# Performance work log

Measured on AMD Instinct MI355X. Metric: run time of the kernel, lower is better.

## Reference

```python
import jax, jax.numpy as jnp
import numpy as np

B, M, L, IN_C, MID_C, OUT_C = 1, 128, 256, 256, 32, 128


def setup_inputs() -> dict:
    key = jax.random.key(0)
    k_x, k_proj, k_final = jax.random.split(key, 3)
    return {
        "x1d": jax.random.normal(k_x, (B, M, L, IN_C), dtype=jnp.float32),
        "norm_w": jnp.ones((IN_C,), dtype=jnp.float32),
        "norm_b": jnp.zeros((IN_C,), dtype=jnp.float32),
        "proj_w": jax.random.normal(k_proj, (2 * MID_C, IN_C), dtype=jnp.float32) * 0.02,
        "proj_b": jnp.zeros((2 * MID_C,), dtype=jnp.float32),
        "final_w": jax.random.normal(k_final, (OUT_C, MID_C * MID_C), dtype=jnp.float32) * 0.02,
        "final_b": jnp.zeros((OUT_C,), dtype=jnp.float32),
    }


def reference(x1d, norm_w, norm_b, proj_w, proj_b, final_w, final_b):
    # LayerNorm over channel dim
    mu = jnp.mean(x1d, axis=-1, keepdims=True)
    var = jnp.mean(jnp.square(x1d - mu), axis=-1, keepdims=True)
    x = (x1d - mu) * jax.lax.rsqrt(var + 1e-5) * norm_w + norm_b

    mid_c = proj_w.shape[0] // 2
    # Linear -> (b, m, L, 2*mid_c); view (..., mid_c, 2); chunk & squeeze:
    # i = interleaved even channels, j = interleaved odd channels
    p = jnp.einsum('bmlc,dc->bmld', x, proj_w) + proj_b
    p = p.reshape(*p.shape[:-1], mid_c, 2)
    i, j = p[..., 0], p[..., 1]          # each (b, m, L, mid_c)

    m = x1d.shape[1]
    # Outer product mean over the MSA (m) dimension -> (b, L, L, mid_c, mid_c)
    x2d = jnp.einsum('bmix,bmjy->bijxy', i, j) / m

    b, li, lj = x2d.shape[0], x2d.shape[1], x2d.shape[2]
    flat = x2d.reshape(b, li, lj, mid_c * mid_c)
    out = jnp.einsum('bijf,of->bijo', flat, final_w) + final_b
    return out
```

## Files before the change

### kernel.cpp

```cpp
#include <hip/hip_runtime.h>
#include <hip/hip_bf16.h>

#define DEVINL __device__ __forceinline__

typedef float  f32x4_t  __attribute__((ext_vector_type(4)));
typedef float  f32x16_t __attribute__((ext_vector_type(16)));
typedef short  bf16x8_t __attribute__((ext_vector_type(8)));

#define MFMA16(a,b,c) __builtin_amdgcn_mfma_f32_16x16x32_bf16((a),(b),(c),0,0,0)
#define MFMA32(a,b,c) __builtin_amdgcn_mfma_f32_32x32x16_bf16((a),(b),(c),0,0,0)

DEVINL unsigned short f2bf(float f) {
  union { float f; unsigned u; } v; v.f = f;
  unsigned r = v.u + 0x7fffu + ((v.u >> 16) & 1u);
  return (unsigned short)(r >> 16);
}

DEVINL unsigned pk2bf(float lo, float hi) {
  union { __hip_bfloat162 h2; unsigned u; } v;
  v.h2 = __float22bfloat162_rn(make_float2(lo, hi));
  return v.u;
}


__global__ __launch_bounds__(256) void kA(const float* __restrict__ x,
                                          const float* __restrict__ nw,
                                          const float* __restrict__ nb,
                                          const float* __restrict__ pw,
                                          const float* __restrict__ pb,
                                          const float* __restrict__ fw,
                                          unsigned short* __restrict__ Wb,
                                          unsigned short* __restrict__ Ig,
                                          unsigned short* __restrict__ Jg) {
  if (blockIdx.x >= 1024) {
    int T = (blockIdx.x - 1024) * 256 + threadIdx.x;
    int o     = T >> 8;
    int kpos0 = (T & 255) * 4;
    int y  = kpos0 >> 5;
    int x0 = kpos0 & 31;
    const float* fo = fw + o * 1024 + y;
    ushort4 u;
    u.x = f2bf(fo[(x0 + 0) * 32]);
    u.y = f2bf(fo[(x0 + 1) * 32]);
    u.z = f2bf(fo[(x0 + 2) * 32]);
    u.w = f2bf(fo[(x0 + 3) * 32]);
    size_t off = (size_t)((o >> 5) * 64 + (kpos0 >> 4)) * 512 + (o & 31) * 16
               + ((kpos0 >> 3) & 1) * 8 + (kpos0 & 7);
    *(ushort4*)&Wb[off] = u;
    return;
  }
  __shared__ unsigned short xnl[32 * 264];
  __shared__ unsigned short pwl[64 * 264];
  __shared__ unsigned short ep[64 * 36];
  const int tid  = threadIdx.x;
  const int wv   = tid >> 6;
  const int lane = tid & 63;
  const int q    = lane >> 4;
  const int ln16 = lane & 15;
  const int l    = blockIdx.x & 255;
  const int m0   = (blockIdx.x >> 8) * 32;

  const float4* xs = (const float4*)x;
  float4 v[8];
#pragma unroll
  for (int i = 0; i < 8; i++) {
    int row = m0 + i * 4 + wv;
    v[i] = xs[row * 16384 + l * 64 + lane];
  }
  float4 nw4 = ((const float4*)nw)[lane];
  float4 nb4 = ((const float4*)nb)[lane];

#pragma unroll
  for (int i = 0; i < 8; i++) {
    float s  = v[i].x + v[i].y + v[i].z + v[i].w;
    float ss = v[i].x * v[i].x + v[i].y * v[i].y + v[i].z * v[i].z + v[i].w * v[i].w;
#pragma unroll
    for (int off = 32; off > 0; off >>= 1) {
      s  += __shfl_xor(s, off);
      ss += __shfl_xor(ss, off);
    }
    float mu  = s * (1.0f / 256.0f);
    float var = ss * (1.0f / 256.0f) - mu * mu;
    float rs  = rsqrtf(var + 1e-5f);
    ushort4 u;
    u.x = f2bf((v[i].x - mu) * rs * nw4.x + nb4.x);
    u.y = f2bf((v[i].y - mu) * rs * nw4.y + nb4.y);
    u.z = f2bf((v[i].z - mu) * rs * nw4.z + nb4.z);
    u.w = f2bf((v[i].w - mu) * rs * nw4.w + nb4.w);
    *(ushort4*)&xnl[(i * 4 + wv) * 264 + lane * 4] = u;
  }

  const float4* ps = (const float4*)pw;
#pragma unroll
  for (int i = 0; i < 16; i++) {
    float4 w4 = ps[i * 256 + tid];
    ushort4 u;
    u.x = f2bf(w4.x); u.y = f2bf(w4.y); u.z = f2bf(w4.z); u.w = f2bf(w4.w);
    *(ushort4*)&pwl[(i * 4 + wv) * 264 + lane * 4] = u;
  }
  __syncthreads();

  const int rt = wv & 1;
  const int db = (wv >> 1) * 32;
  f32x4_t acc[2] = {{0.f, 0.f, 0.f, 0.f}, {0.f, 0.f, 0.f, 0.f}};
#pragma unroll
  for (int kc = 0; kc < 8; kc++) {
    bf16x8_t a  = *(const bf16x8_t*)&xnl[(rt * 16 + ln16) * 264 + kc * 32 + q * 8];
    bf16x8_t b0 = *(const bf16x8_t*)&pwl[(db + ln16) * 264 + kc * 32 + q * 8];
    bf16x8_t b1 = *(const bf16x8_t*)&pwl[(db + 16 + ln16) * 264 + kc * 32 + q * 8];
    acc[0] = MFMA16(a, b0, acc[0]);
    acc[1] = MFMA16(a, b1, acc[1]);
  }

#pragma unroll
  for (int t2 = 0; t2 < 2; t2++) {
    int d = db + t2 * 16 + ln16;
    float bias  = pb[d];
    float scale = (d & 1) ? 1.0f : (1.0f / 128.0f);
#pragma unroll
    for (int r = 0; r < 4; r++) {
      int mloc = rt * 16 + q * 4 + r;
      ep[d * 36 + mloc] = f2bf((acc[t2][r] + bias) * scale);
    }
  }
  __syncthreads();

  const int h  = tid >> 3;
  const int m4 = tid & 7;
  const size_t off = (size_t)(l * 8 + (m0 >> 4) + (m4 >> 2)) * 512 + h * 16 + ((m4 >> 1) & 1) * 8 + (m4 & 1) * 4;
  ushort4 vi = *(const ushort4*)&ep[(2 * h) * 36 + m4 * 4];
  *(ushort4*)&Ig[off] = vi;
  ushort4 vj = *(const ushort4*)&ep[(2 * h + 1) * 36 + m4 * 4];
  *(ushort4*)&Jg[off] = vj;
}

__global__ __launch_bounds__(512, 2) void kB(const unsigned short* __restrict__ Ig,
                                             const unsigned short* __restrict__ Jg,
                                             const unsigned short* __restrict__ Wb,
                                             const float* __restrict__ fb,
                                             float* __restrict__ out) {
  extern __shared__ unsigned short fl[];
  constexpr int P = 1048;
  const int tid  = threadIdx.x;
  const int w    = tid >> 6;
  const int lane = tid & 63;
  const int ln32 = lane & 31;
  const int h    = lane >> 5;
  const int p    = blockIdx.x >> 4;
  const int t    = blockIdx.x & 15;

  bf16x8_t jb[2][8];
  const size_t jbase = (size_t)(t * 16 + 2 * w) * 4096 + ln32 * 16 + h * 8;
#pragma unroll
  for (int mc = 0; mc < 8; mc++) jb[0][mc] = *(const bf16x8_t*)&Jg[jbase + mc * 512];
#pragma unroll
  for (int mc = 0; mc < 8; mc++) jb[1][mc] = *(const bf16x8_t*)&Jg[jbase + 4096 + mc * 512];

#pragma unroll
  for (int s = 0; s < 2; s++) {
    const int jl = 2 * w + s;
#pragma unroll
    for (int ilp = 0; ilp < 2; ilp++) {
      bf16x8_t af[2][8];
#pragma unroll
      for (int u = 0; u < 2; u++)
#pragma unroll
        for (int mc = 0; mc < 8; mc++)
          af[u][mc] = *(const bf16x8_t*)&Ig[(size_t)((p * 4 + ilp * 2 + u) * 8 + mc) * 512 + ln32 * 16 + h * 8];
      f32x16_t c[2];
#pragma unroll
      for (int i = 0; i < 16; i++) { c[0][i] = 0.f; c[1][i] = 0.f; }
#pragma unroll
      for (int mc = 0; mc < 8; mc++) {
        c[0] = MFMA32(af[0][mc], jb[s][mc], c[0]);
        c[1] = MFMA32(af[1][mc], jb[s][mc], c[1]);
      }
#pragma unroll
      for (int u = 0; u < 2; u++) {
        unsigned short* fr = &fl[((ilp * 2 + u) * 16 + jl) * P];
#pragma unroll
        for (int g = 0; g < 4; g++) {
          int cp = (4 * ln32 + g) ^ (ln32 & 7);
          uint2 pv;
          pv.x = pk2bf(c[u][4 * g + 0], c[u][4 * g + 1]);
          pv.y = pk2bf(c[u][4 * g + 2], c[u][4 * g + 3]);
          *(uint2*)&fr[cp * 8 + h * 4] = pv;
        }
      }
    }
  }

  const int ot = w & 3;
  const int kh = w >> 2;
  const unsigned short* Wp = Wb + (size_t)(ot * 64 + kh * 32) * 512 + ln32 * 16 + h * 8;
  bf16x8_t bq[4];
  bq[0] = *(const bf16x8_t*)&Wp[0];
  bq[1] = *(const bf16x8_t*)&Wp[512];

  __syncthreads();

  bq[2] = *(const bf16x8_t*)&Wp[2 * 512];
  bq[3] = *(const bf16x8_t*)&Wp[3 * 512];

#define LDA(rt, kc) (*(const bf16x8_t*)&fl[((rt) * 32 + ln32) * P + \
    ((((kh * 32 + (kc)) * 2 + h) ^ (((kh * 32 + (kc)) >> 1) & 7)) * 8)])

  f32x16_t o2[2];
#pragma unroll
  for (int i = 0; i < 16; i++) { o2[0][i] = 0.f; o2[1][i] = 0.f; }

  bf16x8_t a0 = LDA(0, 0), a1 = LDA(1, 0);
#pragma unroll
  for (int kc = 0; kc < 32; kc++) {
    bf16x8_t ac0 = a0, ac1 = a1, bc = bq[kc & 3];
    if (kc < 31) { a0 = LDA(0, kc + 1); a1 = LDA(1, kc + 1); }
    if (kc < 28) bq[kc & 3] = *(const bf16x8_t*)&Wp[(kc + 4) * 512];
    o2[0] = MFMA32(ac0, bc, o2[0]);
    o2[1] = MFMA32(ac1, bc, o2[1]);
  }
#undef LDA

  __syncthreads();
  float* red = (float*)fl;
  if (kh == 1) {
#pragma unroll
    for (int rt = 0; rt < 2; rt++) {
      float* bb = red + (ot * 2 + rt) * 1024 + lane * 2;
#pragma unroll
      for (int k = 0; k < 8; k++)
        *(float2*)&bb[k * 128] = make_float2(o2[rt][2 * k], o2[rt][2 * k + 1]);
    }
  }
  __syncthreads();
  if (kh == 0) {
    const float bias = fb[ot * 32 + ln32];
    float* ob = out + ((size_t)(p * 4) * 256 + t * 16) * 128 + ot * 32 + ln32;
#pragma unroll
    for (int rt = 0; rt < 2; rt++) {
      const float* bb = red + (ot * 2 + rt) * 1024 + lane * 2;
#pragma unroll
      for (int k = 0; k < 8; k++) {
        float2 rv = *(const float2*)&bb[k * 128];
        int r0 = 2 * k, r1 = 2 * k + 1;
        int br0 = rt * 32 + (r0 & 3) + 8 * (r0 >> 2) + 4 * h;
        int br1 = rt * 32 + (r1 & 3) + 8 * (r1 >> 2) + 4 * h;
        ob[(br0 >> 4) * 32768 + (br0 & 15) * 128] = o2[rt][r0] + rv.x + bias;
        ob[(br1 >> 4) * 32768 + (br1 & 15) * 128] = o2[rt][r1] + rv.y + bias;
      }
    }
  }
}

extern "C" void kernel_launch(void* const* d_in, const int* in_sizes, int n_in,
                              void* d_out, int out_size, void* d_ws, size_t ws_size,
                              hipStream_t stream) {
  const float* x1d     = (const float*)d_in[0];
  const float* norm_w  = (const float*)d_in[1];
  const float* norm_b  = (const float*)d_in[2];
  const float* proj_w  = (const float*)d_in[3];
  const float* proj_b  = (const float*)d_in[4];
  const float* final_w = (const float*)d_in[5];
  const float* final_b = (const float*)d_in[6];
  float* outp          = (float*)d_out;

  unsigned short* Wb  = (unsigned short*)d_ws;
  unsigned short* Igp = Wb + 131072;
  unsigned short* Jgp = Igp + 1048576;

  const int kb_lds = 64 * 1048 * 2;
  hipFuncSetAttribute((const void*)kB, hipFuncAttributeMaxDynamicSharedMemorySize, kb_lds);

  kA<<<1152, 256, 0, stream>>>(x1d, norm_w, norm_b, proj_w, proj_b, final_w, Wb, Igp, Jgp);
  kB<<<1024, 512, kb_lds, stream>>>(Igp, Jgp, Wb, final_b, outp);
}
```

Before: 136.8 us.

## Split outer-product stage by j parity to overlap with final projection GEMM

The first GEMM (outer product into shared memory) is split into even and odd j halves, with a barrier between them. The final-projection GEMM on the even half can then start while other warps finish the odd half, instead of waiting behind a single barrier. The second GEMM's warp split moves from 4 output tiles × 2 K halves to 2 output pairs × 4 K quarters. Each A fragment read from LDS now feeds two MFMAs, which cuts LDS traffic per MFMA. In exchange there are more barriers, a 4-way cross-warp reduction through shared memory, and more live accumulator registers.

Measured after the change: 156.4 us. 1.14x slower.

```diff
diff --git a/kernel.cpp b/kernel.cpp
--- a/kernel.cpp
+++ b/kernel.cpp
@@ -149,16 +149,10 @@
   const int p    = blockIdx.x >> 4;
   const int t    = blockIdx.x & 15;
 
-  bf16x8_t jb[2][8];
-  const size_t jbase = (size_t)(t * 16 + 2 * w) * 4096 + ln32 * 16 + h * 8;
-#pragma unroll
-  for (int mc = 0; mc < 8; mc++) jb[0][mc] = *(const bf16x8_t*)&Jg[jbase + mc * 512];
-#pragma unroll
-  for (int mc = 0; mc < 8; mc++) jb[1][mc] = *(const bf16x8_t*)&Jg[jbase + 4096 + mc * 512];
-
-#pragma unroll
-  for (int s = 0; s < 2; s++) {
-    const int jl = 2 * w + s;
+  const unsigned short* Ibase = Ig + (size_t)(p * 32) * 512 + ln32 * 16 + h * 8;
+  const unsigned short* Jb    = Jg + (size_t)(t * 16) * 4096 + ln32 * 16 + h * 8;
+
+  auto gemm1 = [&](int jl, const bf16x8_t* jb) {
 #pragma unroll
     for (int ilp = 0; ilp < 2; ilp++) {
       bf16x8_t af[2][8];
@@ -166,14 +160,14 @@
       for (int u = 0; u < 2; u++)
 #pragma unroll
         for (int mc = 0; mc < 8; mc++)
-          af[u][mc] = *(const bf16x8_t*)&Ig[(size_t)((p * 4 + ilp * 2 + u) * 8 + mc) * 512 + ln32 * 16 + h * 8];
+          af[u][mc] = *(const bf16x8_t*)&Ibase[(size_t)((ilp * 2 + u) * 8 + mc) * 512];
       f32x16_t c[2];
 #pragma unroll
       for (int i = 0; i < 16; i++) { c[0][i] = 0.f; c[1][i] = 0.f; }
 #pragma unroll
       for (int mc = 0; mc < 8; mc++) {
-        c[0] = MFMA32(af[0][mc], jb[s][mc], c[0]);
-        c[1] = MFMA32(af[1][mc], jb[s][mc], c[1]);
+        c[0] = MFMA32(af[0][mc], jb[mc], c[0]);
+        c[1] = MFMA32(af[1][mc], jb[mc], c[1]);
       }
 #pragma unroll
       for (int u = 0; u < 2; u++) {
@@ -188,66 +182,104 @@
         }
       }
     }
-  }
-
-  const int ot = w & 3;
-  const int kh = w >> 2;
-  const unsigned short* Wp = Wb + (size_t)(ot * 64 + kh * 32) * 512 + ln32 * 16 + h * 8;
-  bf16x8_t bq[4];
-  bq[0] = *(const bf16x8_t*)&Wp[0];
-  bq[1] = *(const bf16x8_t*)&Wp[512];
-
-  __syncthreads();
-
-  bq[2] = *(const bf16x8_t*)&Wp[2 * 512];
-  bq[3] = *(const bf16x8_t*)&Wp[3 * 512];
-
-#define LDA(rt, kc) (*(const bf16x8_t*)&fl[((rt) * 32 + ln32) * P + \
-    ((((kh * 32 + (kc)) * 2 + h) ^ (((kh * 32 + (kc)) >> 1) & 7)) * 8)])
-
-  f32x16_t o2[2];
-#pragma unroll
-  for (int i = 0; i < 16; i++) { o2[0][i] = 0.f; o2[1][i] = 0.f; }
-
-  bf16x8_t a0 = LDA(0, 0), a1 = LDA(1, 0);
-#pragma unroll
-  for (int kc = 0; kc < 32; kc++) {
-    bf16x8_t ac0 = a0, ac1 = a1, bc = bq[kc & 3];
-    if (kc < 31) { a0 = LDA(0, kc + 1); a1 = LDA(1, kc + 1); }
-    if (kc < 28) bq[kc & 3] = *(const bf16x8_t*)&Wp[(kc + 4) * 512];
-    o2[0] = MFMA32(ac0, bc, o2[0]);
-    o2[1] = MFMA32(ac1, bc, o2[1]);
-  }
-#undef LDA
-
-  __syncthreads();
+  };
+
+  const int ow = w & 1;
+  const int kq = w >> 1;
+  const unsigned short* Wp = Wb + ((size_t)(ow * 2) * 64 + kq * 16) * 512 + ln32 * 16 + h * 8;
+  const unsigned short* ar0 = &fl[((ln32 >> 3) * 16 + 2 * (ln32 & 7)) * P];
+
+  auto gemm2h = [&](int par, f32x16_t& d0, f32x16_t& d1, bf16x8_t wr[2][4]) {
+    const unsigned short* ar = ar0 + par * P;
+    auto lda = [&](int kc) {
+      int K16 = kq * 16 + kc;
+      int c2  = K16 * 2 + h;
+      int cps = c2 ^ ((K16 >> 1) & 7);
+      return *(const bf16x8_t*)&ar[cps * 8];
+    };
+    bf16x8_t a0 = lda(0), a1 = lda(1);
+#pragma unroll
+    for (int kc = 0; kc < 16; kc++) {
+      bf16x8_t ac = a0;
+      a0 = a1;
+      if (kc < 14) a1 = lda(kc + 2);
+      bf16x8_t b0 = wr[0][kc & 3], b1 = wr[1][kc & 3];
+      if (kc < 12) {
+        wr[0][kc & 3] = *(const bf16x8_t*)&Wp[(kc + 4) * 512];
+        wr[1][kc & 3] = *(const bf16x8_t*)&Wp[32768 + (kc + 4) * 512];
+      }
+      d0 = MFMA32(ac, b0, d0);
+      d1 = MFMA32(ac, b1, d1);
+    }
+  };
+
+  bf16x8_t jbE[8], jbO[8];
+#pragma unroll
+  for (int mc = 0; mc < 8; mc++) jbE[mc] = *(const bf16x8_t*)&Jb[(size_t)(2 * w) * 4096 + mc * 512];
+#pragma unroll
+  for (int mc = 0; mc < 8; mc++) jbO[mc] = *(const bf16x8_t*)&Jb[(size_t)(2 * w + 1) * 4096 + mc * 512];
+
+  gemm1(2 * w, jbE);
+
+  bf16x8_t wr[2][4];
+#pragma unroll
+  for (int d = 0; d < 4; d++) {
+    wr[0][d] = *(const bf16x8_t*)&Wp[d * 512];
+    wr[1][d] = *(const bf16x8_t*)&Wp[32768 + d * 512];
+  }
+  __syncthreads();
+
+  gemm1(2 * w + 1, jbO);
+
+  f32x16_t oE0, oE1, oO0, oO1;
+#pragma unroll
+  for (int i = 0; i < 16; i++) { oE0[i] = 0.f; oE1[i] = 0.f; oO0[i] = 0.f; oO1[i] = 0.f; }
+  gemm2h(0, oE0, oE1, wr);
+
+#pragma unroll
+  for (int d = 0; d < 4; d++) {
+    wr[0][d] = *(const bf16x8_t*)&Wp[d * 512];
+    wr[1][d] = *(const bf16x8_t*)&Wp[32768 + d * 512];
+  }
+  __syncthreads();
+
+  gemm2h(1, oO0, oO1, wr);
+  __syncthreads();
+
   float* red = (float*)fl;
-  if (kh == 1) {
-#pragma unroll
-    for (int rt = 0; rt < 2; rt++) {
-      float* bb = red + (ot * 2 + rt) * 1024 + lane * 2;
-#pragma unroll
-      for (int k = 0; k < 8; k++)
-        *(float2*)&bb[k * 128] = make_float2(o2[rt][2 * k], o2[rt][2 * k + 1]);
-    }
-  }
-  __syncthreads();
-  if (kh == 0) {
-    const float bias = fb[ot * 32 + ln32];
-    float* ob = out + ((size_t)(p * 4) * 256 + t * 16) * 128 + ot * 32 + ln32;
-#pragma unroll
-    for (int rt = 0; rt < 2; rt++) {
-      const float* bb = red + (ot * 2 + rt) * 1024 + lane * 2;
-#pragma unroll
-      for (int k = 0; k < 8; k++) {
-        float2 rv = *(const float2*)&bb[k * 128];
-        int r0 = 2 * k, r1 = 2 * k + 1;
-        int br0 = rt * 32 + (r0 & 3) + 8 * (r0 >> 2) + 4 * h;
-        int br1 = rt * 32 + (r1 & 3) + 8 * (r1 >> 2) + 4 * h;
-        ob[(br0 >> 4) * 32768 + (br0 & 15) * 128] = o2[rt][r0] + rv.x + bias;
-        ob[(br1 >> 4) * 32768 + (br1 & 15) * 128] = o2[rt][r1] + rv.y + bias;
-      }
-    }
+  if (kq > 0) {
+    const int part = kq - 1;
+#pragma unroll
+    for (int par = 0; par < 2; par++)
+#pragma unroll
+      for (int ots = 0; ots < 2; ots++) {
+        const f32x16_t& d = par ? (ots ? oO1 : oO0) : (ots ? oE1 : oE0);
+        float* bb = red + part * 8192 + par * 4096 + (ow * 2 + ots) * 32 + ln32;
+#pragma unroll
+        for (int r = 0; r < 16; r++) {
+          int rr = (r & 3) + 8 * (r >> 2) + 4 * h;
+          bb[rr * 128] = d[r];
+        }
+      }
+  }
+  __syncthreads();
+  if (kq == 0) {
+#pragma unroll
+    for (int par = 0; par < 2; par++)
+#pragma unroll
+      for (int ots = 0; ots < 2; ots++) {
+        const f32x16_t& d = par ? (ots ? oO1 : oO0) : (ots ? oE1 : oE0);
+        const int o = (ow * 2 + ots) * 32 + ln32;
+        const float bias = fb[o];
+        const float* bb = red + par * 4096 + (ow * 2 + ots) * 32 + ln32;
+#pragma unroll
+        for (int r = 0; r < 16; r++) {
+          int rr = (r & 3) + 8 * (r >> 2) + 4 * h;
+          float val = d[r] + bias + bb[rr * 128] + bb[8192 + rr * 128] + bb[16384 + rr * 128];
+          int il = rr >> 3, jl = 2 * (rr & 7) + par;
+          out[((size_t)(p * 4 + il) * 256 + t * 16 + jl) * 128 + o] = val;
+        }
+      }
   }
 }
 
```

## Warp-specialize kB into producer/consumer waves with double-buffered LDS tiles

Applied to the files above, without the earlier changes.

Restructures the second kernel so four waves compute outer-product tiles into a double-buffered LDS region while the other four waves run the final projection GEMM on the previous tile. The grid shrinks from 1024 to 256 blocks, and each block loops over 8 j-tiles, keeping the I fragments in registers across iterations. The goal is to overlap the two GEMM stages and amortize I loads, removing the split-K reduction through LDS. The cost is fewer blocks, so less parallelism across CUs, plus per-iteration barriers that could serialize the two stages if they are unbalanced.

After: 249.7 us. +82.6%, slower.

```diff
diff --git a/kernel.cpp b/kernel.cpp
--- a/kernel.cpp
+++ b/kernel.cpp
@@ -140,113 +140,97 @@
                                              const float* __restrict__ fb,
                                              float* __restrict__ out) {
   extern __shared__ unsigned short fl[];
-  constexpr int P = 1048;
   const int tid  = threadIdx.x;
   const int w    = tid >> 6;
   const int lane = tid & 63;
   const int ln32 = lane & 31;
   const int h    = lane >> 5;
-  const int p    = blockIdx.x >> 4;
-  const int t    = blockIdx.x & 15;
-
-  bf16x8_t jb[2][8];
-  const size_t jbase = (size_t)(t * 16 + 2 * w) * 4096 + ln32 * 16 + h * 8;
-#pragma unroll
-  for (int mc = 0; mc < 8; mc++) jb[0][mc] = *(const bf16x8_t*)&Jg[jbase + mc * 512];
-#pragma unroll
-  for (int mc = 0; mc < 8; mc++) jb[1][mc] = *(const bf16x8_t*)&Jg[jbase + 4096 + mc * 512];
-
-#pragma unroll
-  for (int s = 0; s < 2; s++) {
-    const int jl = 2 * w + s;
-#pragma unroll
-    for (int ilp = 0; ilp < 2; ilp++) {
-      bf16x8_t af[2][8];
-#pragma unroll
-      for (int u = 0; u < 2; u++)
-#pragma unroll
-        for (int mc = 0; mc < 8; mc++)
-          af[u][mc] = *(const bf16x8_t*)&Ig[(size_t)((p * 4 + ilp * 2 + u) * 8 + mc) * 512 + ln32 * 16 + h * 8];
-      f32x16_t c[2];
-#pragma unroll
-      for (int i = 0; i < 16; i++) { c[0][i] = 0.f; c[1][i] = 0.f; }
-#pragma unroll
-      for (int mc = 0; mc < 8; mc++) {
-        c[0] = MFMA32(af[0][mc], jb[s][mc], c[0]);
-        c[1] = MFMA32(af[1][mc], jb[s][mc], c[1]);
-      }
-#pragma unroll
-      for (int u = 0; u < 2; u++) {
-        unsigned short* fr = &fl[((ilp * 2 + u) * 16 + jl) * P];
-#pragma unroll
-        for (int g = 0; g < 4; g++) {
-          int cp = (4 * ln32 + g) ^ (ln32 & 7);
-          uint2 pv;
-          pv.x = pk2bf(c[u][4 * g + 0], c[u][4 * g + 1]);
-          pv.y = pk2bf(c[u][4 * g + 2], c[u][4 * g + 3]);
-          *(uint2*)&fr[cp * 8 + h * 4] = pv;
+  const int p    = blockIdx.x >> 2;
+  const int g    = blockIdx.x & 3;
+
+  if (w < 4) {
+    bf16x8_t af[4][8];
+#pragma unroll
+    for (int il = 0; il < 4; il++)
+#pragma unroll
+      for (int mc = 0; mc < 8; mc++)
+        af[il][mc] = *(const bf16x8_t*)&Ig[(size_t)((p * 4 + il) * 8 + mc) * 512 + ln32 * 16 + h * 8];
+
+    for (int k = 0; k < 8; k++) {
+      unsigned short* buf = fl + (k & 1) * 32768;
+      const int t8 = g * 8 + k;
+#pragma unroll
+      for (int s = 0; s < 2; s++) {
+        const int jll = w * 2 + s;
+        const unsigned short* Jb = Jg + (size_t)(t8 * 8 + jll) * 4096 + ln32 * 16 + h * 8;
+        bf16x8_t jb[8];
+#pragma unroll
+        for (int mc = 0; mc < 8; mc++) jb[mc] = *(const bf16x8_t*)&Jb[mc * 512];
+#pragma unroll
+        for (int il = 0; il < 4; il++) {
+          f32x16_t c;
+#pragma unroll
+          for (int i = 0; i < 16; i++) c[i] = 0.f;
+#pragma unroll
+          for (int mc = 0; mc < 8; mc++) c = MFMA32(af[il][mc], jb[mc], c);
+          const int row = il * 8 + jll;
+          unsigned short* fr = buf + row * 1024;
+#pragma unroll
+          for (int g4 = 0; g4 < 4; g4++) {
+            int cc = 4 * ln32 + g4;
+            int cp = cc ^ ((cc >> 2) & 7) ^ (row & 7);
+            uint2 pv;
+            pv.x = pk2bf(c[4 * g4 + 0], c[4 * g4 + 1]);
+            pv.y = pk2bf(c[4 * g4 + 2], c[4 * g4 + 3]);
+            *(uint2*)&fr[cp * 8 + h * 4] = pv;
+          }
         }
       }
-    }
-  }
-
-  const int ot = w & 3;
-  const int kh = w >> 2;
-  const unsigned short* Wp = Wb + (size_t)(ot * 64 + kh * 32) * 512 + ln32 * 16 + h * 8;
-  bf16x8_t bq[4];
-  bq[0] = *(const bf16x8_t*)&Wp[0];
-  bq[1] = *(const bf16x8_t*)&Wp[512];
-
-  __syncthreads();
-
-  bq[2] = *(const bf16x8_t*)&Wp[2 * 512];
-  bq[3] = *(const bf16x8_t*)&Wp[3 * 512];
-
-#define LDA(rt, kc) (*(const bf16x8_t*)&fl[((rt) * 32 + ln32) * P + \
-    ((((kh * 32 + (kc)) * 2 + h) ^ (((kh * 32 + (kc)) >> 1) & 7)) * 8)])
-
-  f32x16_t o2[2];
-#pragma unroll
-  for (int i = 0; i < 16; i++) { o2[0][i] = 0.f; o2[1][i] = 0.f; }
-
-  bf16x8_t a0 = LDA(0, 0), a1 = LDA(1, 0);
-#pragma unroll
-  for (int kc = 0; kc < 32; kc++) {
-    bf16x8_t ac0 = a0, ac1 = a1, bc = bq[kc & 3];
-    if (kc < 31) { a0 = LDA(0, kc + 1); a1 = LDA(1, kc + 1); }
-    if (kc < 28) bq[kc & 3] = *(const bf16x8_t*)&Wp[(kc + 4) * 512];
-    o2[0] = MFMA32(ac0, bc, o2[0]);
-    o2[1] = MFMA32(ac1, bc, o2[1]);
-  }
-#undef LDA
-
-  __syncthreads();
-  float* red = (float*)fl;
-  if (kh == 1) {
-#pragma unroll
-    for (int rt = 0; rt < 2; rt++) {
-      float* bb = red + (ot * 2 + rt) * 1024 + lane * 2;
-#pragma unroll
-      for (int k = 0; k < 8; k++)
-        *(float2*)&bb[k * 128] = make_float2(o2[rt][2 * k], o2[rt][2 * k + 1]);
-    }
-  }
-  __syncthreads();
-  if (kh == 0) {
+      __syncthreads();
+    }
+    __syncthreads();
+  } else {
+    const int ot = w - 4;
+    const unsigned short* Wp = Wb + (size_t)(ot * 64) * 512 + ln32 * 16 + h * 8;
     const float bias = fb[ot * 32 + ln32];
-    float* ob = out + ((size_t)(p * 4) * 256 + t * 16) * 128 + ot * 32 + ln32;
-#pragma unroll
-    for (int rt = 0; rt < 2; rt++) {
-      const float* bb = red + (ot * 2 + rt) * 1024 + lane * 2;
-#pragma unroll
-      for (int k = 0; k < 8; k++) {
-        float2 rv = *(const float2*)&bb[k * 128];
-        int r0 = 2 * k, r1 = 2 * k + 1;
-        int br0 = rt * 32 + (r0 & 3) + 8 * (r0 >> 2) + 4 * h;
-        int br1 = rt * 32 + (r1 & 3) + 8 * (r1 >> 2) + 4 * h;
-        ob[(br0 >> 4) * 32768 + (br0 & 15) * 128] = o2[rt][r0] + rv.x + bias;
-        ob[(br1 >> 4) * 32768 + (br1 & 15) * 128] = o2[rt][r1] + rv.y + bias;
+    __syncthreads();
+    for (int k = 1; k <= 8; k++) {
+      const unsigned short* buf = fl + ((k - 1) & 1) * 32768;
+      const unsigned short* A0  = buf + ln32 * 1024;
+      auto lda = [&](int K16) {
+        int c  = 2 * K16 + h;
+        int cp = c ^ ((c >> 2) & 7) ^ (ln32 & 7);
+        return *(const bf16x8_t*)&A0[cp * 8];
+      };
+      f32x16_t o0, o1;
+#pragma unroll
+      for (int i = 0; i < 16; i++) { o0[i] = 0.f; o1[i] = 0.f; }
+      bf16x8_t ar[2][2], br[2][2];
+      ar[0][0] = lda(0);  br[0][0] = *(const bf16x8_t*)&Wp[0];
+      ar[1][0] = lda(32); br[1][0] = *(const bf16x8_t*)&Wp[32 * 512];
+      ar[0][1] = lda(1);  br[0][1] = *(const bf16x8_t*)&Wp[1 * 512];
+      ar[1][1] = lda(33); br[1][1] = *(const bf16x8_t*)&Wp[33 * 512];
+#pragma unroll
+      for (int K = 0; K < 32; K++) {
+        bf16x8_t a0 = ar[0][K & 1], b0 = br[0][K & 1];
+        bf16x8_t a1 = ar[1][K & 1], b1 = br[1][K & 1];
+        if (K < 30) {
+          ar[0][K & 1] = lda(K + 2);
+          br[0][K & 1] = *(const bf16x8_t*)&Wp[(K + 2) * 512];
+          ar[1][K & 1] = lda(K + 34);
+          br[1][K & 1] = *(const bf16x8_t*)&Wp[(K + 34) * 512];
+        }
+        o0 = MFMA32(a0, b0, o0);
+        o1 = MFMA32(a1, b1, o1);
       }
+      const int t8 = g * 8 + (k - 1);
+      float* ob = out + ((size_t)(p * 4) * 256 + t8 * 8) * 128 + ot * 32 + ln32;
+#pragma unroll
+      for (int r = 0; r < 16; r++) {
+        int rr = (r & 3) + 8 * (r >> 2) + 4 * h;
+        ob[((rr >> 3) * 256 + (rr & 7)) * 128] = o0[r] + o1[r] + bias;
+      }
+      __syncthreads();
     }
   }
 }
@@ -267,9 +251,9 @@
   unsigned short* Igp = Wb + 131072;
   unsigned short* Jgp = Igp + 1048576;
 
-  const int kb_lds = 64 * 1048 * 2;
+  const int kb_lds = 2 * 32 * 1024 * 2;
   hipFuncSetAttribute((const void*)kB, hipFuncAttributeMaxDynamicSharedMemorySize, kb_lds);
 
   kA<<<1152, 256, 0, stream>>>(x1d, norm_w, norm_b, proj_w, proj_b, final_w, Wb, Igp, Jgp);
-  kB<<<1024, 512, kb_lds, stream>>>(Igp, Jgp, Wb, final_b, outp);
-}
+  kB<<<256, 512, kb_lds, stream>>>(Igp, Jgp, Wb, final_b, outp);
+}
```
